# Performance work log

Measured on AMD Instinct MI355X. Metric: run time of the kernel, lower is better.

The kernel has to match this reference:

```python
import jax, jax.numpy as jnp
import numpy as np
from jax import lax

N_SRC = 2
K_BASES = 8
N_ITER = 5
NMF_EPS = 1e-20
IP_EPS = 1e-20


def setup_inputs() -> dict:
    key = jax.random.key(0)
    kx, kt, kv = jax.random.split(key, 3)
    M, J, I = 2, 2048, 1025
    X = jax.random.normal(kx, (M, J, I, 2), dtype=jnp.float32)
    T0 = jax.random.uniform(kt, (I, K_BASES, N_SRC), dtype=jnp.float32,
                            minval=1e-08, maxval=1.0)
    V0 = jax.random.uniform(kv, (K_BASES, J, N_SRC), dtype=jnp.float32,
                            minval=1e-08, maxval=1.0)
    return {"X": X, "T0": T0, "V0": V0}


def _nmf_update(Tn, Vn, Yn, eps):
    # Tn: (I,K), Vn: (K,J), Yn: (I,J) complex
    Rn = Tn @ Vn
    magR = jnp.abs(Rn)
    YdR = jnp.abs(Yn) ** 2 / (magR ** 2 + eps)   # |Y|^2 / R^2
    Rd = 1.0 / (magR + eps)
    Tn = Tn * jnp.sqrt((YdR @ Vn.T) / (Rd @ Vn.T + eps))
    Rn = Tn @ Vn
    Rd2 = 1.0 / (jnp.abs(Rn) + eps)
    Vn = Vn * jnp.sqrt((Tn.T @ YdR) / (Tn.T @ Rd2 + eps))
    return Tn, Vn, Tn @ Vn


def _ilrma(X, T0, V0):
    M, J, I, _ = X.shape
    N = N_SRC
    # view_as_complex(X.permute(2,0,1,3)) -> (I, M, J) complex
    Xc = (X[..., 0] + 1j * X[..., 1]).astype(jnp.complex64).transpose(2, 0, 1)
    eye_M = jnp.eye(M, dtype=jnp.complex64)
    W0 = jnp.broadcast_to(jnp.eye(N, M, dtype=jnp.complex64), (I, N, M))
    Y0 = jnp.einsum('inm,imj->inj', W0, Xc)

    def one_iter(carry, _):
        W, T, V, Y = carry
        for n in range(N):  # N=2, structurally distinct small loop
            Tn, Vn, Rn = _nmf_update(T[:, :, n], V[:, :, n], Y[:, n, :], NMF_EPS)
            T = T.at[:, :, n].set(Tn)
            V = V.at[:, :, n].set(Vn)
            # batched per-frequency-bin IP update (vectorizes torch's loop over i)
            inv_Rn = 1.0 / (Rn + IP_EPS)                      # (I,J)
            Xw = Xc * jnp.sqrt(inv_Rn)[:, None, :]            # (I,M,J)
            D = jnp.einsum('imj,ikj->imk', Xw, Xw.conj()) / J  # (I,M,M)
            Dreg = D + IP_EPS * eye_M
            A = jnp.einsum('inm,imk->ink', W, Dreg)           # (I,N,M), N==M
            e_n = eye_M[:, n]                                  # (M,)
            b = jnp.linalg.solve(A, jnp.broadcast_to(e_n, (I, M))[..., None])[..., 0]  # (I,M)
            Db = jnp.einsum('imk,ik->im', Dreg, b)
            denom = jnp.sqrt(jnp.real(jnp.einsum('im,im->i', b.conj(), Db)) + IP_EPS)
            W = W.at[:, n, :].set((b / denom[:, None]).conj())
        Y = jnp.einsum('inm,imj->inj', W, Xc)
        return (W, T, V, Y), None

    (W, T, V, Y), _ = lax.scan(one_iter, (W0, T0, V0, Y0), None, length=N_ITER)
    out = Y.transpose(1, 2, 0)                 # (N, J, I)
    return jnp.stack([out.real, out.imag], axis=-1)  # view_as_real -> (N,J,I,2)


def reference(X, T0, V0):
    return _ilrma(X, T0, V0)
```

## Files before the change

kernel.cpp:

```cpp
#include <hip/hip_runtime.h>

#define I_DIM 1025
#define J_DIM 2048
#define K_B 8
#define IC 33
#define EPSF 1e-20f


__device__ __forceinline__ int rev4i(int x) {
  return ((x & 1) << 3) | ((x & 2) << 1) | ((x & 4) >> 1) | ((x & 8) >> 3);
}
__device__ __forceinline__ int rev3i(int x) {
  return ((x & 1) << 2) | (x & 2) | ((x & 4) >> 2);
}

__device__ __forceinline__ void foldReduce16(float* vals, int lane) {
  #pragma unroll
  for (int step = 0; step < 4; ++step) {
    const int nv = 8 >> step;
    const int bit = (lane >> step) & 1;
    #pragma unroll
    for (int q = 0; q < nv; ++q) {
      float a = vals[q], b = vals[q + nv];
      float send = bit ? a : b;
      float keep = bit ? b : a;
      vals[q] = keep + __shfl_xor(send, 1 << step);
    }
  }
  vals[0] += __shfl_xor(vals[0], 16);
  vals[0] += __shfl_xor(vals[0], 32);
}

__device__ __forceinline__ void foldReduce8(float* vals, int lane) {
  #pragma unroll
  for (int step = 0; step < 3; ++step) {
    const int nv = 4 >> step;
    const int bit = (lane >> step) & 1;
    #pragma unroll
    for (int q = 0; q < nv; ++q) {
      float a = vals[q], b = vals[q + nv];
      float send = bit ? a : b;
      float keep = bit ? b : a;
      vals[q] = keep + __shfl_xor(send, 1 << step);
    }
  }
  vals[0] += __shfl_xor(vals[0], 8);
  vals[0] += __shfl_xor(vals[0], 16);
  vals[0] += __shfl_xor(vals[0], 32);
}

__device__ __forceinline__ float2 cmul(float2 a, float2 b) {
  return make_float2(a.x*b.x - a.y*b.y, a.x*b.y + a.y*b.x);
}
__device__ __forceinline__ float2 cadd(float2 a, float2 b) {
  return make_float2(a.x + b.x, a.y + b.y);
}
__device__ __forceinline__ float2 csub(float2 a, float2 b) {
  return make_float2(a.x - b.x, a.y - b.y);
}
__device__ __forceinline__ float2 cdiv(float2 a, float2 b) {
  float s = 1.0f / (b.x*b.x + b.y*b.y);
  return make_float2((a.x*b.x + a.y*b.y)*s, (a.y*b.x - a.x*b.y)*s);
}

__global__ __launch_bounds__(256) void k_tr_init(
    const float* __restrict__ X, float4* __restrict__ Xq,
    const float* __restrict__ T0, const float* __restrict__ V0,
    float* __restrict__ T, float* __restrict__ V, float* __restrict__ W)
{
  const int tx = threadIdx.x, ty = threadIdx.y;
  const int lt = ty * 32 + tx;
  const int bid = blockIdx.y * 33 + blockIdx.x;
  int t = bid * 256 + lt;
  if (t < 2 * K_B * J_DIM) {
    int n = t >> 14;
    int r = t & 16383;
    int j = r >> 3, k = r & 7;
    V[t] = V0[(k * J_DIM + j) * 2 + n];
  }
  if (t < 2 * I_DIM * K_B) {
    int n = t / (I_DIM * K_B);
    int r = t % (I_DIM * K_B);
    int i = r / K_B, k = r % K_B;
    T[t] = T0[(i * K_B + k) * 2 + n];
  }
  if (t < I_DIM * 8) {
    int u = t & 7;
    int c = u & 1, m = (u >> 1) & 1, n = u >> 2;
    W[t] = (n == m && c == 0) ? 1.0f : 0.0f;
  }
  __shared__ float t0r[32][33], t0i[32][33], t1r[32][33], t1i[32][33];
  const int i0 = blockIdx.x * 32, j0 = blockIdx.y * 32;
  const float2* __restrict__ X2 = (const float2*)X;
  #pragma unroll
  for (int jj = 0; jj < 4; ++jj) {
    int jl = ty + jj * 8;
    int i = i0 + tx;
    if (i < I_DIM) {
      float2 v0 = X2[(size_t)(0 * J_DIM + j0 + jl) * I_DIM + i];
      float2 v1 = X2[(size_t)(1 * J_DIM + j0 + jl) * I_DIM + i];
      t0r[jl][tx] = v0.x; t0i[jl][tx] = v0.y;
      t1r[jl][tx] = v1.x; t1i[jl][tx] = v1.y;
    }
  }
  __syncthreads();
  #pragma unroll
  for (int ii = 0; ii < 4; ++ii) {
    int il = ty + ii * 8;
    int i = i0 + il;
    if (i < I_DIM) {
      Xq[(size_t)i * J_DIM + j0 + tx] =
        make_float4(t0r[tx][il], t0i[tx][il], t1r[tx][il], t1i[tx][il]);
    }
  }
}

template<int N>
__device__ __forceinline__ void nmfT_body(
    int i, int tid,
    const float4* __restrict__ Xq,
    float* __restrict__ T, const float* __restrict__ V,
    const float* __restrict__ W, float* __restrict__ YdR)
{
  float4 xs[8];
  #pragma unroll
  for (int u = 0; u < 8; ++u) xs[u] = Xq[(size_t)i * J_DIM + u * 256 + tid];

  const float4 w = ((const float4*)W)[i * 2 + N];
  float t[K_B];
  const int trow = (N * I_DIM + i) * K_B;
  #pragma unroll
  for (int k = 0; k < K_B; ++k) t[k] = T[trow + k];

  float num[K_B], den[K_B];
  #pragma unroll
  for (int k = 0; k < K_B; ++k) { num[k] = 0.f; den[k] = 0.f; }

  const float4* __restrict__ V4 = (const float4*)V;
  #pragma unroll
  for (int u = 0; u < 8; ++u) {
    int j = u * 256 + tid;
    float4 va = V4[(N * J_DIM + j) * 2 + 0];
    float4 vb = V4[(N * J_DIM + j) * 2 + 1];
    float v[K_B] = {va.x, va.y, va.z, va.w, vb.x, vb.y, vb.z, vb.w};
    float rn = 0.f;
    #pragma unroll
    for (int k = 0; k < K_B; ++k) rn += t[k] * v[k];
    float4 x = xs[u];
    float yr = w.x * x.x - w.y * x.y + w.z * x.z - w.w * x.w;
    float yi = w.x * x.y + w.y * x.x + w.z * x.w + w.w * x.z;
    float rd = 1.0f / (fabsf(rn) + EPSF);
    float ydr = (yr * yr + yi * yi) * rd * rd;
    YdR[(size_t)i * J_DIM + j] = ydr;
    #pragma unroll
    for (int k = 0; k < K_B; ++k) { num[k] += ydr * v[k]; den[k] += rd * v[k]; }
  }

  float vals[16];
  #pragma unroll
  for (int k = 0; k < K_B; ++k) { vals[k] = num[k]; vals[K_B + k] = den[k]; }
  const int wave = tid >> 6, lane = tid & 63;
  foldReduce16(vals, lane);
  __shared__ float redT[4][16];
  if (lane < 16) redT[wave][lane] = vals[0];
  __syncthreads();
  if (tid < K_B) {
    int r = rev4i(tid);
    float nm = redT[0][r] + redT[1][r] + redT[2][r] + redT[3][r];
    float dn = redT[0][r+1] + redT[1][r+1] + redT[2][r+1] + redT[3][r+1];
    T[trow + tid] *= sqrtf(nm / (dn + EPSF));
  }
}

__device__ __forceinline__ void ip_solve_both(
    int i,
    float D000, float p0, float q0, float D110,
    float D001, float p1, float q1, float D111,
    float* __restrict__ W)
{
  float4 w0 = ((const float4*)W)[i * 2 + 0];
  float4 w1 = ((const float4*)W)[i * 2 + 1];
  float2 W00 = make_float2(w0.x, w0.y), W01 = make_float2(w0.z, w0.w);
  float2 W10 = make_float2(w1.x, w1.y), W11 = make_float2(w1.z, w1.w);
  {
    float D00 = D000 + EPSF, D11 = D110 + EPSF;
    float2 D01 = make_float2(p0, q0);
    float2 D10 = make_float2(p0, -q0);
    float2 A00 = cadd(make_float2(W00.x * D00, W00.y * D00), cmul(W01, D10));
    float2 A01 = cadd(cmul(W00, D01), make_float2(W01.x * D11, W01.y * D11));
    float2 A10 = cadd(make_float2(W10.x * D00, W10.y * D00), cmul(W11, D10));
    float2 A11 = cadd(cmul(W10, D01), make_float2(W11.x * D11, W11.y * D11));
    float2 det = csub(cmul(A00, A11), cmul(A01, A10));
    float2 b0 = cdiv(A11, det);
    float2 b1 = cdiv(make_float2(-A10.x, -A10.y), det);
    float2 Db0 = cadd(make_float2(D00 * b0.x, D00 * b0.y), cmul(D01, b1));
    float2 Db1 = cadd(cmul(D10, b0), make_float2(D11 * b1.x, D11 * b1.y));
    float ip = b0.x * Db0.x + b0.y * Db0.y + b1.x * Db1.x + b1.y * Db1.y;
    float inv = 1.0f / sqrtf(ip + EPSF);
    W00 = make_float2(b0.x * inv, -b0.y * inv);
    W01 = make_float2(b1.x * inv, -b1.y * inv);
  }
  {
    float D00 = D001 + EPSF, D11 = D111 + EPSF;
    float2 D01 = make_float2(p1, q1);
    float2 D10 = make_float2(p1, -q1);
    float2 A00 = cadd(make_float2(W00.x * D00, W00.y * D00), cmul(W01, D10));
    float2 A01 = cadd(cmul(W00, D01), make_float2(W01.x * D11, W01.y * D11));
    float2 A10 = cadd(make_float2(W10.x * D00, W10.y * D00), cmul(W11, D10));
    float2 A11 = cadd(cmul(W10, D01), make_float2(W11.x * D11, W11.y * D11));
    float2 det = csub(cmul(A00, A11), cmul(A01, A10));
    float2 b0 = cdiv(make_float2(-A01.x, -A01.y), det);
    float2 b1 = cdiv(A00, det);
    float2 Db0 = cadd(make_float2(D00 * b0.x, D00 * b0.y), cmul(D01, b1));
    float2 Db1 = cadd(cmul(D10, b0), make_float2(D11 * b1.x, D11 * b1.y));
    float ip = b0.x * Db0.x + b0.y * Db0.y + b1.x * Db1.x + b1.y * Db1.y;
    float inv = 1.0f / sqrtf(ip + EPSF);
    W10 = make_float2(b0.x * inv, -b0.y * inv);
    W11 = make_float2(b1.x * inv, -b1.y * inv);
  }
  ((float4*)W)[i * 2 + 0] = make_float4(W00.x, W00.y, W01.x, W01.y);
  ((float4*)W)[i * 2 + 1] = make_float4(W10.x, W10.y, W11.x, W11.y);
}

template<int N>
__device__ __forceinline__ void part_body(
    int pb, int tid,
    const float* __restrict__ T, const float* __restrict__ V,
    const float* __restrict__ YdR,
    float* __restrict__ Pn, float* __restrict__ Pd)
{
  const int jb = pb & 7;
  const int c  = pb >> 3;
  const int j  = jb * 256 + tid;
  const int i0 = c * 32;
  const int ni = min(32, I_DIM - i0);
  __shared__ float sT[32 * K_B];
  if (tid < ni * K_B) sT[tid] = T[(N * I_DIM + i0) * K_B + tid];
  __syncthreads();
  const float4* __restrict__ V4 = (const float4*)V;
  float4 va = V4[(N * J_DIM + j) * 2 + 0];
  float4 vb = V4[(N * J_DIM + j) * 2 + 1];
  float v[K_B] = {va.x, va.y, va.z, va.w, vb.x, vb.y, vb.z, vb.w};
  float num[K_B], den[K_B];
  #pragma unroll
  for (int k = 0; k < K_B; ++k) { num[k] = 0.f; den[k] = 0.f; }

  if (ni == 32) {
    #pragma unroll
    for (int g = 0; g < 4; ++g) {
      float yd[8];
      #pragma unroll
      for (int q = 0; q < 8; ++q)
        yd[q] = YdR[(size_t)(i0 + g * 8 + q) * J_DIM + j];
      #pragma unroll
      for (int q = 0; q < 8; ++q) {
        const int ii = g * 8 + q;
        float rn = 0.f;
        #pragma unroll
        for (int k = 0; k < K_B; ++k) rn += sT[ii * K_B + k] * v[k];
        float rd2 = 1.0f / (fabsf(rn) + EPSF);
        #pragma unroll
        for (int k = 0; k < K_B; ++k) {
          num[k] += sT[ii * K_B + k] * yd[q];
          den[k] += sT[ii * K_B + k] * rd2;
        }
      }
    }
  } else {
    for (int ii = 0; ii < ni; ++ii) {
      float ydr = YdR[(size_t)(i0 + ii) * J_DIM + j];
      float rn = 0.f;
      #pragma unroll
      for (int k = 0; k < K_B; ++k) rn += sT[ii * K_B + k] * v[k];
      float rd2 = 1.0f / (fabsf(rn) + EPSF);
      #pragma unroll
      for (int k = 0; k < K_B; ++k) {
        num[k] += sT[ii * K_B + k] * ydr;
        den[k] += sT[ii * K_B + k] * rd2;
      }
    }
  }
  ((float4*)Pn)[((size_t)c * J_DIM + j) * 2 + 0] = make_float4(num[0], num[1], num[2], num[3]);
  ((float4*)Pn)[((size_t)c * J_DIM + j) * 2 + 1] = make_float4(num[4], num[5], num[6], num[7]);
  ((float4*)Pd)[((size_t)c * J_DIM + j) * 2 + 0] = make_float4(den[0], den[1], den[2], den[3]);
  ((float4*)Pd)[((size_t)c * J_DIM + j) * 2 + 1] = make_float4(den[4], den[5], den[6], den[7]);
}

template<int N>
__device__ __forceinline__ void fin_body(
    int fb, int tid, float* __restrict__ V,
    const float* __restrict__ Pn, const float* __restrict__ Pd)
{
  const int t = fb * 256 + tid;
  float nm = 0.f, dn = 0.f;
  #pragma unroll
  for (int c = 0; c < IC; ++c) {
    nm += Pn[(size_t)c * (K_B * J_DIM) + t];
    dn += Pd[(size_t)c * (K_B * J_DIM) + t];
  }
  V[N * (K_B * J_DIM) + t] *= sqrtf(nm / (dn + EPSF));
}

__global__ __launch_bounds__(256) void k_nmf2(
    const float4* __restrict__ Xq, float* __restrict__ T,
    const float* __restrict__ V, const float* __restrict__ W,
    float* __restrict__ YdR0, float* __restrict__ YdR1)
{
  int b = blockIdx.x;
  int p, pop;
  if (b >= 2048) { p = 1024; pop = b - 2048; }
  else { pop = (b >> 3) & 1; p = ((b >> 4) << 3) | (b & 7); }
  if (pop == 0)
    nmfT_body<0>(p, threadIdx.x, Xq, T, V, W, YdR0);
  else
    nmfT_body<1>(p, threadIdx.x, Xq, T, V, W, YdR1);
}

__global__ __launch_bounds__(256) void k_part2(
    const float* __restrict__ T, const float* __restrict__ V,
    const float* __restrict__ Y0, const float* __restrict__ Y1,
    float* __restrict__ Pn0, float* __restrict__ Pd0,
    float* __restrict__ Pn1, float* __restrict__ Pd1)
{
  if (blockIdx.x < 264)
    part_body<0>(blockIdx.x, threadIdx.x, T, V, Y0, Pn0, Pd0);
  else
    part_body<1>(blockIdx.x - 264, threadIdx.x, T, V, Y1, Pn1, Pd1);
}

__global__ __launch_bounds__(256) void k_fin2(
    float* __restrict__ V,
    const float* __restrict__ Pn0, const float* __restrict__ Pd0,
    const float* __restrict__ Pn1, const float* __restrict__ Pd1)
{
  if (blockIdx.x < 64)
    fin_body<0>(blockIdx.x, threadIdx.x, V, Pn0, Pd0);
  else
    fin_body<1>(blockIdx.x - 64, threadIdx.x, V, Pn1, Pd1);
}

__global__ __launch_bounds__(256) void k_ip2(
    const float4* __restrict__ Xq, const float* __restrict__ T,
    const float* __restrict__ V, float* __restrict__ W)
{
  const int i = blockIdx.x;
  const int tid = threadIdx.x;
  float4 xs[8];
  #pragma unroll
  for (int u = 0; u < 8; ++u) xs[u] = Xq[(size_t)i * J_DIM + u * 256 + tid];

  float t0[K_B], t1[K_B];
  #pragma unroll
  for (int k = 0; k < K_B; ++k) {
    t0[k] = T[(0 * I_DIM + i) * K_B + k];
    t1[k] = T[(1 * I_DIM + i) * K_B + k];
  }
  const float4* __restrict__ V4 = (const float4*)V;
  float acc[8];
  #pragma unroll
  for (int q = 0; q < 8; ++q) acc[q] = 0.f;

  #pragma unroll
  for (int u = 0; u < 8; ++u) {
    int j = u * 256 + tid;
    float4 va0 = V4[(0 * J_DIM + j) * 2 + 0];
    float4 vb0 = V4[(0 * J_DIM + j) * 2 + 1];
    float4 va1 = V4[(1 * J_DIM + j) * 2 + 0];
    float4 vb1 = V4[(1 * J_DIM + j) * 2 + 1];
    float rn0 = t0[0]*va0.x + t0[1]*va0.y + t0[2]*va0.z + t0[3]*va0.w
              + t0[4]*vb0.x + t0[5]*vb0.y + t0[6]*vb0.z + t0[7]*vb0.w;
    float rn1 = t1[0]*va1.x + t1[1]*va1.y + t1[2]*va1.z + t1[3]*va1.w
              + t1[4]*vb1.x + t1[5]*vb1.y + t1[6]*vb1.z + t1[7]*vb1.w;
    float w0 = 1.0f / (rn0 + EPSF);
    float w1 = 1.0f / (rn1 + EPSF);
    float4 x = xs[u];
    float m00 = x.x * x.x + x.y * x.y;
    float m11 = x.z * x.z + x.w * x.w;
    float m01r = x.x * x.z + x.y * x.w;
    float m01i = x.y * x.z - x.x * x.w;
    acc[0] += m00 * w0; acc[1] += m01r * w0; acc[2] += m01i * w0; acc[3] += m11 * w0;
    acc[4] += m00 * w1; acc[5] += m01r * w1; acc[6] += m01i * w1; acc[7] += m11 * w1;
  }
  const int wave = tid >> 6, lane = tid & 63;
  foldReduce8(acc, lane);
  __shared__ float red[4][8];
  if (lane < 8) red[wave][lane] = acc[0];
  __syncthreads();
  if (tid == 0) {
    const float invJ = 1.0f / (float)J_DIM;
    float s[8];
    #pragma unroll
    for (int vv = 0; vv < 8; ++vv) {
      int r = rev3i(vv);
      s[vv] = (red[0][r] + red[1][r] + red[2][r] + red[3][r]) * invJ;
    }
    ip_solve_both(i, s[0], s[1], s[2], s[3], s[4], s[5], s[6], s[7], W);
  }
}

__global__ __launch_bounds__(256) void k_out(
    const float* __restrict__ X, const float* __restrict__ W, float* __restrict__ out)
{
  const int j = blockIdx.x;
  const int i = blockIdx.y * 256 + threadIdx.x;
  if (i >= I_DIM) return;
  const float2* __restrict__ X2 = (const float2*)X;
  float2 x0 = X2[(size_t)(0 * J_DIM + j) * I_DIM + i];
  float2 x1 = X2[(size_t)(1 * J_DIM + j) * I_DIM + i];
  const float4* __restrict__ W4 = (const float4*)W;
  float4 w0 = W4[i * 2 + 0];
  float4 w1 = W4[i * 2 + 1];
  float2* __restrict__ O = (float2*)out;
  float yr = w0.x * x0.x - w0.y * x0.y + w0.z * x1.x - w0.w * x1.y;
  float yi = w0.x * x0.y + w0.y * x0.x + w0.z * x1.y + w0.w * x1.x;
  O[(size_t)(0 * J_DIM + j) * I_DIM + i] = make_float2(yr, yi);
  yr = w1.x * x0.x - w1.y * x0.y + w1.z * x1.x - w1.w * x1.y;
  yi = w1.x * x0.y + w1.y * x0.x + w1.z * x1.y + w1.w * x1.x;
  O[(size_t)(1 * J_DIM + j) * I_DIM + i] = make_float2(yr, yi);
}

extern "C" void kernel_launch(void* const* d_in, const int* in_sizes, int n_in,
                              void* d_out, int out_size, void* d_ws, size_t ws_size,
                              hipStream_t stream) {
  const float* X  = (const float*)d_in[0];
  const float* T0 = (const float*)d_in[1];
  const float* V0 = (const float*)d_in[2];
  float* ws = (float*)d_ws;
  float4* Xq  = (float4*)ws;
  float* YdR0 = ws + 8396800;
  float* YdR1 = ws + 10496000;
  float* T    = ws + 12595200;
  float* V    = ws + 12611600;
  float* W    = ws + 12644368;
  float* Pn0  = ws + 12652568;
  float* Pd0  = ws + 13193240;
  float* Pn1  = ws + 13733912;
  float* Pd1  = ws + 14274584;
  float* out  = (float*)d_out;

  k_tr_init<<<dim3(33, 64), dim3(32, 8), 0, stream>>>(X, Xq, T0, V0, T, V, W);
  for (int it = 0; it < 5; ++it) {
    k_nmf2<<<2 * I_DIM, 256, 0, stream>>>(Xq, T, V, W, YdR0, YdR1);
    k_part2<<<2 * 264, 256, 0, stream>>>(T, V, YdR0, YdR1, Pn0, Pd0, Pn1, Pd1);
    k_fin2<<<2 * 64, 256, 0, stream>>>(V, Pn0, Pd0, Pn1, Pd1);
    k_ip2<<<I_DIM, 256, 0, stream>>>(Xq, T, V, W);
  }
  k_out<<<dim3(J_DIM, 5), 256, 0, stream>>>(X, W, out);
}
```

Before: 292.8 us.

## Use packed float2 math, fast reciprocal, and float4 partial-sum finalization

Rewrites the inner loops of the NMF T update, the partial V reduction and the IP covariance kernel around 2-wide float vectors, so the compiler can emit packed FP32 instructions (v_pk_fma_f32). Exact divisions become the hardware approximate reciprocal. The V finalization reads partials as float4 and launches a quarter as many blocks. The goal is fewer ALU instructions and wider memory accesses, at the cost of a slightly less accurate reciprocal and fewer blocks in the small finalization kernel.

```diff
diff --git a/kernel.cpp b/kernel.cpp
--- a/kernel.cpp
+++ b/kernel.cpp
@@ -5,6 +5,8 @@
 #define K_B 8
 #define IC 33
 #define EPSF 1e-20f
+
+typedef float vf2 __attribute__((ext_vector_type(2)));
 
 
 __device__ __forceinline__ int rev4i(int x) {
@@ -127,14 +129,14 @@
   for (int u = 0; u < 8; ++u) xs[u] = Xq[(size_t)i * J_DIM + u * 256 + tid];
 
   const float4 w = ((const float4*)W)[i * 2 + N];
-  float t[K_B];
   const int trow = (N * I_DIM + i) * K_B;
-  #pragma unroll
-  for (int k = 0; k < K_B; ++k) t[k] = T[trow + k];
-
-  float num[K_B], den[K_B];
-  #pragma unroll
-  for (int k = 0; k < K_B; ++k) { num[k] = 0.f; den[k] = 0.f; }
+  vf2 t2[4];
+  #pragma unroll
+  for (int q = 0; q < 4; ++q) t2[q] = vf2{T[trow + 2*q], T[trow + 2*q + 1]};
+
+  vf2 num2[4], den2[4];
+  #pragma unroll
+  for (int q = 0; q < 4; ++q) { num2[q] = vf2{0.f,0.f}; den2[q] = vf2{0.f,0.f}; }
 
   const float4* __restrict__ V4 = (const float4*)V;
   #pragma unroll
@@ -142,23 +144,27 @@
     int j = u * 256 + tid;
     float4 va = V4[(N * J_DIM + j) * 2 + 0];
     float4 vb = V4[(N * J_DIM + j) * 2 + 1];
-    float v[K_B] = {va.x, va.y, va.z, va.w, vb.x, vb.y, vb.z, vb.w};
-    float rn = 0.f;
-    #pragma unroll
-    for (int k = 0; k < K_B; ++k) rn += t[k] * v[k];
+    vf2 v2[4] = {vf2{va.x,va.y}, vf2{va.z,va.w}, vf2{vb.x,vb.y}, vf2{vb.z,vb.w}};
+    vf2 rn2 = t2[0]*v2[0] + t2[1]*v2[1] + t2[2]*v2[2] + t2[3]*v2[3];
+    float rn = rn2.x + rn2.y;
     float4 x = xs[u];
     float yr = w.x * x.x - w.y * x.y + w.z * x.z - w.w * x.w;
     float yi = w.x * x.y + w.y * x.x + w.z * x.w + w.w * x.z;
-    float rd = 1.0f / (fabsf(rn) + EPSF);
+    float rd = __builtin_amdgcn_rcpf(fabsf(rn) + EPSF);
     float ydr = (yr * yr + yi * yi) * rd * rd;
     YdR[(size_t)i * J_DIM + j] = ydr;
+    vf2 ydr2 = vf2{ydr, ydr};
+    vf2 rdv2 = vf2{rd, rd};
     #pragma unroll
-    for (int k = 0; k < K_B; ++k) { num[k] += ydr * v[k]; den[k] += rd * v[k]; }
+    for (int q = 0; q < 4; ++q) { num2[q] += ydr2 * v2[q]; den2[q] += rdv2 * v2[q]; }
   }
 
   float vals[16];
   #pragma unroll
-  for (int k = 0; k < K_B; ++k) { vals[k] = num[k]; vals[K_B + k] = den[k]; }
+  for (int q = 0; q < 4; ++q) {
+    vals[2*q] = num2[q].x;   vals[2*q+1] = num2[q].y;
+    vals[8+2*q] = den2[q].x; vals[8+2*q+1] = den2[q].y;
+  }
   const int wave = tid >> 6, lane = tid & 63;
   foldReduce16(vals, lane);
   __shared__ float redT[4][16];
@@ -234,16 +240,16 @@
   const int j  = jb * 256 + tid;
   const int i0 = c * 32;
   const int ni = min(32, I_DIM - i0);
-  __shared__ float sT[32 * K_B];
-  if (tid < ni * K_B) sT[tid] = T[(N * I_DIM + i0) * K_B + tid];
+  __shared__ float4 sT4[32 * 2];
+  if (tid < ni * 2) sT4[tid] = ((const float4*)(T + (size_t)(N * I_DIM + i0) * K_B))[tid];
   __syncthreads();
   const float4* __restrict__ V4 = (const float4*)V;
   float4 va = V4[(N * J_DIM + j) * 2 + 0];
   float4 vb = V4[(N * J_DIM + j) * 2 + 1];
-  float v[K_B] = {va.x, va.y, va.z, va.w, vb.x, vb.y, vb.z, vb.w};
-  float num[K_B], den[K_B];
-  #pragma unroll
-  for (int k = 0; k < K_B; ++k) { num[k] = 0.f; den[k] = 0.f; }
+  vf2 v2[4] = {vf2{va.x,va.y}, vf2{va.z,va.w}, vf2{vb.x,vb.y}, vf2{vb.z,vb.w}};
+  vf2 num2[4], den2[4];
+  #pragma unroll
+  for (int q = 0; q < 4; ++q) { num2[q] = vf2{0.f,0.f}; den2[q] = vf2{0.f,0.f}; }
 
   if (ni == 32) {
     #pragma unroll
@@ -255,35 +261,39 @@
       #pragma unroll
       for (int q = 0; q < 8; ++q) {
         const int ii = g * 8 + q;
-        float rn = 0.f;
+        float4 ta = sT4[ii * 2], tb = sT4[ii * 2 + 1];
+        vf2 t2[4] = {vf2{ta.x,ta.y}, vf2{ta.z,ta.w}, vf2{tb.x,tb.y}, vf2{tb.z,tb.w}};
+        vf2 rn2 = t2[0]*v2[0] + t2[1]*v2[1] + t2[2]*v2[2] + t2[3]*v2[3];
+        float rd2 = __builtin_amdgcn_rcpf(fabsf(rn2.x + rn2.y) + EPSF);
+        vf2 yd2 = vf2{yd[q], yd[q]};
+        vf2 rdv = vf2{rd2, rd2};
         #pragma unroll
-        for (int k = 0; k < K_B; ++k) rn += sT[ii * K_B + k] * v[k];
-        float rd2 = 1.0f / (fabsf(rn) + EPSF);
-        #pragma unroll
-        for (int k = 0; k < K_B; ++k) {
-          num[k] += sT[ii * K_B + k] * yd[q];
-          den[k] += sT[ii * K_B + k] * rd2;
+        for (int k = 0; k < 4; ++k) {
+          num2[k] += t2[k] * yd2;
+          den2[k] += t2[k] * rdv;
         }
       }
     }
   } else {
     for (int ii = 0; ii < ni; ++ii) {
       float ydr = YdR[(size_t)(i0 + ii) * J_DIM + j];
-      float rn = 0.f;
+      float4 ta = sT4[ii * 2], tb = sT4[ii * 2 + 1];
+      vf2 t2[4] = {vf2{ta.x,ta.y}, vf2{ta.z,ta.w}, vf2{tb.x,tb.y}, vf2{tb.z,tb.w}};
+      vf2 rn2 = t2[0]*v2[0] + t2[1]*v2[1] + t2[2]*v2[2] + t2[3]*v2[3];
+      float rd2 = __builtin_amdgcn_rcpf(fabsf(rn2.x + rn2.y) + EPSF);
+      vf2 yd2 = vf2{ydr, ydr};
+      vf2 rdv = vf2{rd2, rd2};
       #pragma unroll
-      for (int k = 0; k < K_B; ++k) rn += sT[ii * K_B + k] * v[k];
-      float rd2 = 1.0f / (fabsf(rn) + EPSF);
-      #pragma unroll
-      for (int k = 0; k < K_B; ++k) {
-        num[k] += sT[ii * K_B + k] * ydr;
-        den[k] += sT[ii * K_B + k] * rd2;
+      for (int k = 0; k < 4; ++k) {
+        num2[k] += t2[k] * yd2;
+        den2[k] += t2[k] * rdv;
       }
     }
   }
-  ((float4*)Pn)[((size_t)c * J_DIM + j) * 2 + 0] = make_float4(num[0], num[1], num[2], num[3]);
-  ((float4*)Pn)[((size_t)c * J_DIM + j) * 2 + 1] = make_float4(num[4], num[5], num[6], num[7]);
-  ((float4*)Pd)[((size_t)c * J_DIM + j) * 2 + 0] = make_float4(den[0], den[1], den[2], den[3]);
-  ((float4*)Pd)[((size_t)c * J_DIM + j) * 2 + 1] = make_float4(den[4], den[5], den[6], den[7]);
+  ((float4*)Pn)[((size_t)c * J_DIM + j) * 2 + 0] = make_float4(num2[0].x, num2[0].y, num2[1].x, num2[1].y);
+  ((float4*)Pn)[((size_t)c * J_DIM + j) * 2 + 1] = make_float4(num2[2].x, num2[2].y, num2[3].x, num2[3].y);
+  ((float4*)Pd)[((size_t)c * J_DIM + j) * 2 + 0] = make_float4(den2[0].x, den2[0].y, den2[1].x, den2[1].y);
+  ((float4*)Pd)[((size_t)c * J_DIM + j) * 2 + 1] = make_float4(den2[2].x, den2[2].y, den2[3].x, den2[3].y);
 }
 
 template<int N>
@@ -291,14 +301,25 @@
     int fb, int tid, float* __restrict__ V,
     const float* __restrict__ Pn, const float* __restrict__ Pd)
 {
-  const int t = fb * 256 + tid;
-  float nm = 0.f, dn = 0.f;
+  const int t4 = fb * 256 + tid;
+  const float4* __restrict__ Pn4 = (const float4*)Pn;
+  const float4* __restrict__ Pd4 = (const float4*)Pd;
+  float4 nm = make_float4(0.f, 0.f, 0.f, 0.f);
+  float4 dn = make_float4(0.f, 0.f, 0.f, 0.f);
   #pragma unroll
   for (int c = 0; c < IC; ++c) {
-    nm += Pn[(size_t)c * (K_B * J_DIM) + t];
-    dn += Pd[(size_t)c * (K_B * J_DIM) + t];
-  }
-  V[N * (K_B * J_DIM) + t] *= sqrtf(nm / (dn + EPSF));
+    float4 a = Pn4[(size_t)c * 4096 + t4];
+    float4 b = Pd4[(size_t)c * 4096 + t4];
+    nm.x += a.x; nm.y += a.y; nm.z += a.z; nm.w += a.w;
+    dn.x += b.x; dn.y += b.y; dn.z += b.z; dn.w += b.w;
+  }
+  float4* __restrict__ V4o = (float4*)(V + N * (K_B * J_DIM));
+  float4 v = V4o[t4];
+  v.x *= sqrtf(nm.x / (dn.x + EPSF));
+  v.y *= sqrtf(nm.y / (dn.y + EPSF));
+  v.z *= sqrtf(nm.z / (dn.z + EPSF));
+  v.w *= sqrtf(nm.w / (dn.w + EPSF));
+  V4o[t4] = v;
 }
 
 __global__ __launch_bounds__(256) void k_nmf2(
@@ -333,10 +354,10 @@
     const float* __restrict__ Pn0, const float* __restrict__ Pd0,
     const float* __restrict__ Pn1, const float* __restrict__ Pd1)
 {
-  if (blockIdx.x < 64)
+  if (blockIdx.x < 16)
     fin_body<0>(blockIdx.x, threadIdx.x, V, Pn0, Pd0);
   else
-    fin_body<1>(blockIdx.x - 64, threadIdx.x, V, Pn1, Pd1);
+    fin_body<1>(blockIdx.x - 16, threadIdx.x, V, Pn1, Pd1);
 }
 
 __global__ __launch_bounds__(256) void k_ip2(
@@ -349,16 +370,16 @@
   #pragma unroll
   for (int u = 0; u < 8; ++u) xs[u] = Xq[(size_t)i * J_DIM + u * 256 + tid];
 
-  float t0[K_B], t1[K_B];
-  #pragma unroll
-  for (int k = 0; k < K_B; ++k) {
-    t0[k] = T[(0 * I_DIM + i) * K_B + k];
-    t1[k] = T[(1 * I_DIM + i) * K_B + k];
+  vf2 t0_2[4], t1_2[4];
+  #pragma unroll
+  for (int q = 0; q < 4; ++q) {
+    t0_2[q] = vf2{T[(0 * I_DIM + i) * K_B + 2*q], T[(0 * I_DIM + i) * K_B + 2*q + 1]};
+    t1_2[q] = vf2{T[(1 * I_DIM + i) * K_B + 2*q], T[(1 * I_DIM + i) * K_B + 2*q + 1]};
   }
   const float4* __restrict__ V4 = (const float4*)V;
-  float acc[8];
-  #pragma unroll
-  for (int q = 0; q < 8; ++q) acc[q] = 0.f;
+  vf2 acc2[4];
+  #pragma unroll
+  for (int q = 0; q < 4; ++q) acc2[q] = vf2{0.f, 0.f};
 
   #pragma unroll
   for (int u = 0; u < 8; ++u) {
@@ -367,20 +388,22 @@
     float4 vb0 = V4[(0 * J_DIM + j) * 2 + 1];
     float4 va1 = V4[(1 * J_DIM + j) * 2 + 0];
     float4 vb1 = V4[(1 * J_DIM + j) * 2 + 1];
-    float rn0 = t0[0]*va0.x + t0[1]*va0.y + t0[2]*va0.z + t0[3]*va0.w
-              + t0[4]*vb0.x + t0[5]*vb0.y + t0[6]*vb0.z + t0[7]*vb0.w;
-    float rn1 = t1[0]*va1.x + t1[1]*va1.y + t1[2]*va1.z + t1[3]*va1.w
-              + t1[4]*vb1.x + t1[5]*vb1.y + t1[6]*vb1.z + t1[7]*vb1.w;
-    float w0 = 1.0f / (rn0 + EPSF);
-    float w1 = 1.0f / (rn1 + EPSF);
+    vf2 r0 = t0_2[0]*vf2{va0.x,va0.y} + t0_2[1]*vf2{va0.z,va0.w}
+           + t0_2[2]*vf2{vb0.x,vb0.y} + t0_2[3]*vf2{vb0.z,vb0.w};
+    vf2 r1 = t1_2[0]*vf2{va1.x,va1.y} + t1_2[1]*vf2{va1.z,va1.w}
+           + t1_2[2]*vf2{vb1.x,vb1.y} + t1_2[3]*vf2{vb1.z,vb1.w};
+    float w0 = __builtin_amdgcn_rcpf(r0.x + r0.y + EPSF);
+    float w1 = __builtin_amdgcn_rcpf(r1.x + r1.y + EPSF);
     float4 x = xs[u];
-    float m00 = x.x * x.x + x.y * x.y;
-    float m11 = x.z * x.z + x.w * x.w;
-    float m01r = x.x * x.z + x.y * x.w;
-    float m01i = x.y * x.z - x.x * x.w;
-    acc[0] += m00 * w0; acc[1] += m01r * w0; acc[2] += m01i * w0; acc[3] += m11 * w0;
-    acc[4] += m00 * w1; acc[5] += m01r * w1; acc[6] += m01i * w1; acc[7] += m11 * w1;
-  }
+    vf2 mA = vf2{x.x, x.x} * vf2{x.x, x.z} + vf2{x.y, x.y} * vf2{x.y, x.w};
+    vf2 mB = vf2{x.y, x.z} * vf2{x.z, x.z} + vf2{-x.x, x.w} * vf2{x.w, x.w};
+    acc2[0] += mA * vf2{w0, w0};
+    acc2[1] += mB * vf2{w0, w0};
+    acc2[2] += mA * vf2{w1, w1};
+    acc2[3] += mB * vf2{w1, w1};
+  }
+  float acc[8] = {acc2[0].x, acc2[0].y, acc2[1].x, acc2[1].y,
+                  acc2[2].x, acc2[2].y, acc2[3].x, acc2[3].y};
   const int wave = tid >> 6, lane = tid & 63;
   foldReduce8(acc, lane);
   __shared__ float red[4][8];
@@ -442,7 +465,7 @@
   for (int it = 0; it < 5; ++it) {
     k_nmf2<<<2 * I_DIM, 256, 0, stream>>>(Xq, T, V, W, YdR0, YdR1);
     k_part2<<<2 * 264, 256, 0, stream>>>(T, V, YdR0, YdR1, Pn0, Pd0, Pn1, Pd1);
-    k_fin2<<<2 * 64, 256, 0, stream>>>(V, Pn0, Pd0, Pn1, Pd1);
+    k_fin2<<<2 * 16, 256, 0, stream>>>(V, Pn0, Pd0, Pn1, Pd1);
     k_ip2<<<I_DIM, 256, 0, stream>>>(Xq, T, V, W);
   }
   k_out<<<dim3(J_DIM, 5), 256, 0, stream>>>(X, W, out);
```

Result: no change. 289.8 us (-1.0%).
